# Kernel tuning notes

Hardware: AMD Instinct MI355X
Metric: run time of the kernel (lower is better)

Reference implementation:

```python
import jax, jax.numpy as jnp
import numpy as np
import math

B, S, HID, NH, K_SIG = 8, 8192, 1024, 16, 1024
HD = HID // NH
SCALE = math.sqrt(HD)

def _lin(x, W, b):
    # torch nn.Linear: x @ W.T + b, W is [out, in]
    return jnp.einsum('...i,oi->...o', x, W) + b

def setup_inputs() -> dict:
    key = jax.random.key(0)
    ks = jax.random.split(key, 16)
    hidden_states = jax.random.normal(ks[0], (B, S, HID), jnp.float32)
    # mask with exactly K_SIG ones per row (matches torch padding semantics exactly)
    perm = jax.vmap(lambda k: jax.random.permutation(k, S))(jax.random.split(ks[1], B))
    idx = perm[:, :K_SIG]
    mask = jnp.zeros((B, S), bool).at[jnp.arange(B)[:, None], idx].set(True)
    register_state = jax.random.normal(ks[2], (B, HID), jnp.float32)
    def w(k):
        return jax.random.normal(k, (HID, HID), jnp.float32) * 0.02
    def bvec(k):
        return jax.random.normal(k, (HID,), jnp.float32) * 0.02
    return {
        'hidden_states': hidden_states, 'mask': mask, 'register_state': register_state,
        'Wq': w(ks[3]), 'bq': bvec(ks[4]), 'Wk': w(ks[5]), 'bk': bvec(ks[6]),
        'Wv': w(ks[7]), 'bv': bvec(ks[8]), 'Wo': w(ks[9]), 'bo': bvec(ks[10]),
        'Wrk': w(ks[11]), 'brk': bvec(ks[12]), 'Wrv': w(ks[13]), 'brv': bvec(ks[14]),
    }

def reference(hidden_states, mask, register_state, Wq, bq, Wk, bk, Wv, bv, Wo, bo, Wrk, brk, Wrv, brv):
    # sorted indices of the K_SIG True positions per row (stable argsort puts
    # True (~mask == False) first, in original order)
    idx = jnp.argsort(jnp.logical_not(mask), axis=1, stable=True)[:, :K_SIG]  # [B, K_SIG]
    signal = jnp.take_along_axis(hidden_states, idx[:, :, None], axis=1)      # [B, K_SIG, HID]

    Q = _lin(signal, Wq, bq).reshape(B, K_SIG, NH, HD)
    Kt = _lin(signal, Wk, bk)
    Vt = _lin(signal, Wv, bv)
    Kr = _lin(register_state, Wrk, brk)[:, None, :]
    Vr = _lin(register_state, Wrv, brv)[:, None, :]
    K = jnp.concatenate([Kt, Kr], axis=1).reshape(B, K_SIG + 1, NH, HD)
    V = jnp.concatenate([Vt, Vr], axis=1).reshape(B, K_SIG + 1, NH, HD)

    scores = jnp.einsum('bqhd,bkhd->bhqk', Q, K) / SCALE
    attn = jax.nn.softmax(scores, axis=-1)
    ao = jnp.einsum('bhqk,bkhd->bqhd', attn, V).reshape(B, K_SIG, HID)
    ao = _lin(ao, Wo, bo)

    # scatter back into a copy of hidden_states
    out = hidden_states.at[jnp.arange(B)[:, None], idx].set(ao)
    return out
```

## Files before the change

### kernel.cpp

```cpp
#include <hip/hip_runtime.h>
#include <hip/hip_bf16.h>
#include <math.h>

#define Bc    8
#define Sc    8192
#define HIDc  1024
#define NHc   16
#define HDc   64
#define KSc   1024
#define QSCALE 0.18033688f

typedef __bf16 bf16_t;
typedef __bf16 bf16x8 __attribute__((ext_vector_type(8)));
typedef float  f32x4  __attribute__((ext_vector_type(4)));

#define OFF_IDX   ((size_t)256)
#define OFF_SIG   ((size_t)295168)
#define OFF_WQKV  ((size_t)17072384)
#define OFF_WO    ((size_t)23363840)
#define OFF_QKV   ((size_t)25460992)
#define OFF_KR    ((size_t)75792640)
#define OFF_VR    ((size_t)75809024)
#define OFF_AO    ((size_t)75825408)

__device__ inline void gll16(const bf16_t* g, bf16_t* l) {
  __builtin_amdgcn_global_load_lds(
      (const __attribute__((address_space(1))) void*)g,
      (__attribute__((address_space(3))) void*)l, 16, 0, 0);
}

__global__ __launch_bounds__(256) void front1_kernel(
    const unsigned char* __restrict__ m8, int* __restrict__ idx) {
  __shared__ int shc[256];
  __shared__ int f_sh;
  const int b = blockIdx.x, t = threadIdx.x;
  const unsigned char* raw = m8 + (size_t)b * Sc;
  int c8 = 0;
  for (int i = t; i < Sc; i += 256) c8 += (raw[i] != 0);
  shc[t] = c8;
  __syncthreads();
  for (int s2 = 128; s2 > 0; s2 >>= 1) {
    if (t < s2) shc[t] += shc[t + s2];
    __syncthreads();
  }
  if (t == 0) f_sh = (shc[0] == KSc) ? 1 : 0;
  __syncthreads();
  const int f = f_sh;
  const int* m32 = (const int*)m8;
  const int base = b * Sc + t * 32;
  int c = 0;
  for (int i = 0; i < 32; i++)
    c += f ? (m8[base + i] != 0) : (m32[base + i] != 0);
  shc[t] = c;
  __syncthreads();
  if (t == 0) {
    int run = 0;
    for (int j = 0; j < 256; j++) { int v = shc[j]; shc[j] = run; run += v; }
  }
  __syncthreads();
  int off = b * KSc + shc[t];
  for (int i = 0; i < 32; i++) {
    int on = f ? (m8[base + i] != 0) : (m32[base + i] != 0);
    if (on) { idx[off] = t * 32 + i; off++; }
  }
}

__global__ __launch_bounds__(256) void front2_kernel(
    const float* __restrict__ hidden, const int* __restrict__ idx,
    const float* __restrict__ Wq, const float* __restrict__ Wk,
    const float* __restrict__ Wv, const float* __restrict__ Wo,
    const float* __restrict__ rst,
    const float* __restrict__ Wrk, const float* __restrict__ brk,
    const float* __restrict__ Wrv, const float* __restrict__ brv,
    bf16_t* __restrict__ sig, bf16_t* __restrict__ Wqkv,
    bf16_t* __restrict__ Wob, bf16_t* __restrict__ Krb,
    bf16_t* __restrict__ Vrb) {
  const int bid = blockIdx.x, t = threadIdx.x;
  if (bid < 1024) {
    const int s0 = bid * 8;
    const int b = s0 >> 10;
    float4 v[8];
#pragma unroll
    for (int j = 0; j < 8; j++) {
      const int srow = idx[s0 + j];
      v[j] = *(const float4*)(hidden + ((size_t)b * Sc + srow) * HIDc + t * 4);
    }
#pragma unroll
    for (int j = 0; j < 8; j++) {
      bf16_t* d = sig + (size_t)(s0 + j) * HIDc + t * 4;
      d[0] = (bf16_t)v[j].x; d[1] = (bf16_t)v[j].y;
      d[2] = (bf16_t)v[j].z; d[3] = (bf16_t)v[j].w;
    }
  } else if (bid < 5120) {
    int gid = (bid - 1024) * 256 + t;
    int e4 = gid * 4;
    if (e4 < 3 * 1048576) {
      int sel = e4 >> 20, cc = e4 & 1048575;
      const float* src = sel == 0 ? Wq : (sel == 1 ? Wk : Wv);
      float4 v = *(const float4*)(src + cc);
      bf16_t* d = Wqkv + e4;
      d[0] = (bf16_t)v.x; d[1] = (bf16_t)v.y; d[2] = (bf16_t)v.z; d[3] = (bf16_t)v.w;
    } else {
      int cc = e4 - 3 * 1048576;
      float4 v = *(const float4*)(Wo + cc);
      bf16_t* d = Wob + cc;
      d[0] = (bf16_t)v.x; d[1] = (bf16_t)v.y; d[2] = (bf16_t)v.z; d[3] = (bf16_t)v.w;
    }
  } else {
    const int wid = (bid - 5120) * 4 + (t >> 6);
    const int lane = t & 63;
    const int isV = wid >> 10, j = wid & 1023;
    const float* Wrow = (isV ? Wrv : Wrk) + (size_t)j * HIDc;
    float4 w[4];
#pragma unroll
    for (int i = 0; i < 4; i++) w[i] = ((const float4*)Wrow)[i * 64 + lane];
    const float bias = (isV ? brv : brk)[j];
#pragma unroll
    for (int b = 0; b < 8; b++) {
      const float4* r4 = (const float4*)(rst + (size_t)b * HIDc);
      float s = 0.f;
#pragma unroll
      for (int i = 0; i < 4; i++) {
        float4 r = r4[i * 64 + lane];
        s += w[i].x * r.x + w[i].y * r.y + w[i].z * r.z + w[i].w * r.w;
      }
      s += __shfl_xor(s, 1);  s += __shfl_xor(s, 2);  s += __shfl_xor(s, 4);
      s += __shfl_xor(s, 8);  s += __shfl_xor(s, 16); s += __shfl_xor(s, 32);
      if (lane == 0)
        (isV ? Vrb : Krb)[(size_t)b * HIDc + j] = (bf16_t)(s + bias);
    }
  }
}

__device__ inline void gemm_mainloop(const bf16_t* __restrict__ A,
                                     const bf16_t* __restrict__ Bw,
                                     int tile_m, int tile_n,
                                     bf16_t* As, bf16_t* Bs, f32x4 acc[4][4]) {
  const int t = threadIdx.x, lane = t & 63, w = t >> 6;
  const int wm = w >> 1, wn = w & 1;
  const int r16 = lane & 15, kq = lane >> 4;
  for (int k0 = 0; k0 < 1024; k0 += 32) {
#pragma unroll
    for (int rr = 0; rr < 2; ++rr) {
      int e = rr * 2048 + w * 512 + lane * 8;
      int row = e >> 5, kk = e & 31;
      gll16(A + (size_t)(tile_m + row) * 1024 + k0 + kk, As + rr * 2048 + w * 512);
      gll16(Bw + (size_t)(tile_n + row) * 1024 + k0 + kk, Bs + rr * 2048 + w * 512);
    }
    __syncthreads();
    bf16x8 af[4], bfr[4];
#pragma unroll
    for (int m = 0; m < 4; m++)
      af[m] = *(const bf16x8*)(As + (wm * 64 + m * 16 + r16) * 32 + kq * 8);
#pragma unroll
    for (int n = 0; n < 4; n++)
      bfr[n] = *(const bf16x8*)(Bs + (wn * 64 + n * 16 + r16) * 32 + kq * 8);
#pragma unroll
    for (int m = 0; m < 4; m++)
#pragma unroll
      for (int n = 0; n < 4; n++)
        acc[m][n] = __builtin_amdgcn_mfma_f32_16x16x32_bf16(af[m], bfr[n], acc[m][n], 0, 0, 0);
    __syncthreads();
  }
}

__global__ __launch_bounds__(256) void gemm_qkv_kernel(
    const bf16_t* __restrict__ A, const bf16_t* __restrict__ Bw,
    const float* __restrict__ bq, const float* __restrict__ bk,
    const float* __restrict__ bv, bf16_t* __restrict__ C) {
  __shared__ bf16_t As[128 * 32];
  __shared__ bf16_t Bs[128 * 32];
  const int tile_m = blockIdx.y * 128, tile_n = blockIdx.x * 128;
  f32x4 acc[4][4] = {};
  gemm_mainloop(A, Bw, tile_m, tile_n, As, Bs, acc);
  const int t = threadIdx.x, lane = t & 63, w = t >> 6;
  const int wm = w >> 1, wn = w & 1;
  const int r16 = lane & 15, kq = lane >> 4;
#pragma unroll
  for (int m = 0; m < 4; m++)
#pragma unroll
    for (int n = 0; n < 4; n++) {
      int col = tile_n + wn * 64 + n * 16 + r16;
      int sel = col >> 10, cc = col & 1023;
      float bias = sel == 0 ? bq[cc] : (sel == 1 ? bk[cc] : bv[cc]);
#pragma unroll
      for (int r = 0; r < 4; r++) {
        int row = tile_m + wm * 64 + m * 16 + kq * 4 + r;
        float v = acc[m][n][r] + bias;
        if (sel == 0) v *= QSCALE;
        C[(size_t)row * 3072 + col] = (bf16_t)v;
      }
    }
}

__global__ __launch_bounds__(256) void gemm_ao_kernel(
    const bf16_t* __restrict__ A, const bf16_t* __restrict__ Bw,
    const float* __restrict__ bo, const int* __restrict__ idx,
    float* __restrict__ dout) {
  __shared__ bf16_t As[128 * 32];
  __shared__ bf16_t Bs[128 * 32];
  const int tile_m = blockIdx.y * 128, tile_n = blockIdx.x * 128;
  f32x4 acc[4][4] = {};
  gemm_mainloop(A, Bw, tile_m, tile_n, As, Bs, acc);
  const int t = threadIdx.x, lane = t & 63, w = t >> 6;
  const int wm = w >> 1, wn = w & 1;
  const int r16 = lane & 15, kq = lane >> 4;
#pragma unroll
  for (int m = 0; m < 4; m++)
#pragma unroll
    for (int n = 0; n < 4; n++) {
      int col = tile_n + wn * 64 + n * 16 + r16;
      float bias = bo[col];
#pragma unroll
      for (int r = 0; r < 4; r++) {
        int row = tile_m + wm * 64 + m * 16 + kq * 4 + r;
        float v = acc[m][n][r] + bias;
        int bb = row >> 10;
        int drow = idx[row];
        dout[((size_t)bb * Sc + drow) * HIDc + col] = v;
      }
    }
}

__global__ __launch_bounds__(512) void attn_kernel(
    const bf16_t* __restrict__ QKV, const bf16_t* __restrict__ Krb,
    const bf16_t* __restrict__ Vrb, bf16_t* __restrict__ AO) {
  __shared__ bf16_t Kb[3][4096];
  __shared__ bf16_t Vt[2][4096];
  __shared__ bf16_t Pl[8][2048];
  const int t = threadIdx.x, lane = t & 63, w = t >> 6;
  const int gbk = blockIdx.x;
  const int li = (gbk & 7) * 64 + (gbk >> 3);
  const int qt = li & 3, h = (li >> 2) & 15, b = li >> 6;
  const int r16 = lane & 15, kq = lane >> 4;
  const int qbase = qt * 256 + w * 32;

  const int kK = t >> 3;
  const int dK = ((t & 7) ^ (kK & 7)) * 8;
  const bf16_t* kSrc = QKV + (size_t)(b * KSc + kK) * 3072 + 1024 + h * 64 + dK;
  const int kv8 = t >> 3, dv8 = (t & 7) * 8;
  const int vchunk = kv8 >> 3, voff = kv8 & 7, t7 = t & 7;
  const bf16_t* vSrc = QKV + (size_t)(b * KSc + kv8) * 3072 + 2048 + h * 64 + dv8;

  bf16x8 qf[2][2];
#pragma unroll
  for (int m = 0; m < 2; m++)
#pragma unroll
    for (int kc = 0; kc < 2; kc++)
      qf[m][kc] = *(const bf16x8*)(QKV +
          (size_t)(b * KSc + qbase + m * 16 + r16) * 3072 + h * 64 + kc * 32 + kq * 8);

  f32x4 o[2][4] = {};
  f32x4 osum[2] = {};

  bf16x8 vones;
#pragma unroll
  for (int j = 0; j < 8; j++) vones[j] = (bf16_t)1.0f;

  {
    bf16x8 v0 = *(const bf16x8*)vSrc;
    gll16(kSrc, &Kb[0][w * 512]);
    gll16(kSrc + (size_t)64 * 3072, &Kb[1][w * 512]);
#pragma unroll
    for (int j = 0; j < 8; j++)
      Vt[0][(dv8 + j) * 64 + (((vchunk ^ j ^ t7) << 3) | voff)] = v0[j];
  }
  asm volatile("s_waitcnt vmcnt(1) lgkmcnt(0)" ::: "memory");
  __builtin_amdgcn_s_barrier();

  for (int kt = 0; kt < 17; ++kt) {
    const int cbK = kt % 3;
    const int cbV = kt & 1, nbV = cbV ^ 1;
    bf16x8 vreg = {};
    if (kt < 15) {
      vreg = *(const bf16x8*)(vSrc + (size_t)(kt + 1) * 64 * 3072);
    } else if (kt == 15) {
      if (kv8 == 0) vreg = *(const bf16x8*)(Vrb + (size_t)b * HIDc + h * 64 + dv8);
    }
    if (kt <= 13) {
      gll16(kSrc + (size_t)(kt + 2) * 64 * 3072, &Kb[(kt + 2) % 3][w * 512]);
    } else if (kt == 14) {
      bf16x8 kz = {};
      if (kK == 0) kz = *(const bf16x8*)(Krb + (size_t)b * HIDc + h * 64 + dK);
      *(bf16x8*)(&Kb[1][t * 8]) = kz;
    }
    const bf16_t* Ks = Kb[cbK];

    f32x4 s[2][4] = {};
    __builtin_amdgcn_s_setprio(1);
#pragma unroll
    for (int n = 0; n < 4; n++) {
      const int rowk = n * 16 + r16;
#pragma unroll
      for (int kc = 0; kc < 2; kc++) {
        bf16x8 kf = *(const bf16x8*)(Ks + rowk * 64 +
                                     (((kc * 4 + kq) ^ (rowk & 7)) << 3));
#pragma unroll
        for (int m = 0; m < 2; m++)
          s[m][n] = __builtin_amdgcn_mfma_f32_16x16x32_bf16(kf, qf[m][kc], s[m][n], 0, 0, 0);
      }
    }
    __builtin_amdgcn_s_setprio(0);

    if (kt == 16) {
#pragma unroll
      for (int m = 0; m < 2; m++)
#pragma unroll
        for (int n = 0; n < 4; n++)
#pragma unroll
          for (int r = 0; r < 4; r++)
            if (!(n == 0 && kq == 0 && r == 0)) s[m][n][r] = -1e30f;
    }

    bf16_t* Pw = Pl[w];
#pragma unroll
    for (int m = 0; m < 2; m++)
#pragma unroll
      for (int n = 0; n < 4; n++) {
        float p0 = exp2f(s[m][n][0]), p1 = exp2f(s[m][n][1]);
        float p2 = exp2f(s[m][n][2]), p3 = exp2f(s[m][n][3]);
        unsigned lo, hi;
        asm("v_cvt_pk_bf16_f32 %0, %1, %2" : "=v"(lo) : "v"(p0), "v"(p1));
        asm("v_cvt_pk_bf16_f32 %0, %1, %2" : "=v"(hi) : "v"(p2), "v"(p3));
        unsigned long long pk = (unsigned long long)lo |
                                ((unsigned long long)hi << 32);
        *(unsigned long long*)(Pw + (m * 16 + r16) * 64 +
                               ((n * 16 + kq * 4) ^ ((r16 & 7) << 3))) = pk;
      }

    bf16x8 pa[2][2];
#pragma unroll
    for (int m = 0; m < 2; m++)
#pragma unroll
      for (int kc = 0; kc < 2; kc++)
        pa[m][kc] = *(const bf16x8*)(Pw + (m * 16 + r16) * 64 +
                                     ((kc * 32 + kq * 8) ^ ((r16 & 7) << 3)));

    const bf16_t* Vrow = Vt[cbV];
    __builtin_amdgcn_s_setprio(1);
#pragma unroll
    for (int n = 0; n < 4; n++) {
      const int rowv = n * 16 + r16;
      const int xr = (r16 & 7) ^ ((2 * n + (r16 >> 3)) & 7);
#pragma unroll
      for (int kc = 0; kc < 2; kc++) {
        bf16x8 vb = *(const bf16x8*)(Vrow + rowv * 64 +
                                     (((kc * 4 + kq) ^ xr) << 3));
#pragma unroll
        for (int m = 0; m < 2; m++)
          o[m][n] = __builtin_amdgcn_mfma_f32_16x16x32_bf16(pa[m][kc], vb, o[m][n], 0, 0, 0);
      }
    }
#pragma unroll
    for (int m = 0; m < 2; m++)
#pragma unroll
      for (int kc = 0; kc < 2; kc++)
        osum[m] = __builtin_amdgcn_mfma_f32_16x16x32_bf16(pa[m][kc], vones, osum[m], 0, 0, 0);
    __builtin_amdgcn_s_setprio(0);

    if (kt < 16) {
#pragma unroll
      for (int j = 0; j < 8; j++)
        Vt[nbV][(dv8 + j) * 64 + (((vchunk ^ j ^ t7) << 3) | voff)] = vreg[j];
      asm volatile("s_waitcnt vmcnt(1) lgkmcnt(0)" ::: "memory");
      __builtin_amdgcn_s_barrier();
    }
  }

#pragma unroll
  for (int m = 0; m < 2; m++)
#pragma unroll
    for (int n = 0; n < 4; n++)
#pragma unroll
      for (int r = 0; r < 4; r++) {
        float v = o[m][n][r] / osum[m][r];
        int rowg = b * KSc + qbase + m * 16 + kq * 4 + r;
        int col = h * 64 + n * 16 + r16;
        AO[(size_t)rowg * HIDc + col] = (bf16_t)v;
      }
}

extern "C" void kernel_launch(void* const* d_in, const int* in_sizes, int n_in,
                              void* d_out, int out_size, void* d_ws, size_t ws_size,
                              hipStream_t stream) {
  const float* hidden = (const float*)d_in[0];
  const void*  maskp  = d_in[1];
  const float* rst    = (const float*)d_in[2];
  const float* Wq = (const float*)d_in[3];  const float* bq = (const float*)d_in[4];
  const float* Wk = (const float*)d_in[5];  const float* bk = (const float*)d_in[6];
  const float* Wv = (const float*)d_in[7];  const float* bv = (const float*)d_in[8];
  const float* Wo = (const float*)d_in[9];  const float* bo = (const float*)d_in[10];
  const float* Wrk = (const float*)d_in[11]; const float* brk = (const float*)d_in[12];
  const float* Wrv = (const float*)d_in[13]; const float* brv = (const float*)d_in[14];
  float* dout = (float*)d_out;

  char* ws = (char*)d_ws;
  int*    idx  = (int*)(ws + OFF_IDX);
  bf16_t* sig  = (bf16_t*)(ws + OFF_SIG);
  bf16_t* Wqkv = (bf16_t*)(ws + OFF_WQKV);
  bf16_t* Wob  = (bf16_t*)(ws + OFF_WO);
  bf16_t* QKV  = (bf16_t*)(ws + OFF_QKV);
  bf16_t* Krb  = (bf16_t*)(ws + OFF_KR);
  bf16_t* Vrb  = (bf16_t*)(ws + OFF_VR);
  bf16_t* AO   = (bf16_t*)(ws + OFF_AO);

  hipMemcpyAsync(dout, hidden, (size_t)Bc * Sc * HIDc * sizeof(float),
                 hipMemcpyDeviceToDevice, stream);
  front1_kernel<<<Bc, 256, 0, stream>>>((const unsigned char*)maskp, idx);
  front2_kernel<<<5632, 256, 0, stream>>>(hidden, idx, Wq, Wk, Wv, Wo, rst,
                                          Wrk, brk, Wrv, brv,
                                          sig, Wqkv, Wob, Krb, Vrb);
  gemm_qkv_kernel<<<dim3(24, 64), 256, 0, stream>>>(sig, Wqkv, bq, bk, bv, QKV);
  attn_kernel<<<512, 512, 0, stream>>>(QKV, Krb, Vrb, AO);
  gemm_ao_kernel<<<dim3(8, 64), 256, 0, stream>>>(AO, Wob, bo, idx, dout);
}
```

Measured before the change: 314.2 us.

## Split attention into 256-thread blocks with 128 queries and double-buffered K

Attention blocks shrink from 8 waves over 256 queries to 4 waves over 128 queries, so the grid doubles to 1024 blocks. Each thread now loads two K/V rows per tile, and the K triple buffer becomes a double buffer with a full vmcnt(0) wait each iteration. The aim is more, smaller blocks and less LDS per block so occupancy and load balance improve. In exchange, each K/V tile is loaded by twice as many blocks overall, and the deeper K prefetch is lost.

```diff
diff --git a/kernel.cpp b/kernel.cpp
--- a/kernel.cpp
+++ b/kernel.cpp
@@ -222,25 +222,28 @@
     }
 }
 
-__global__ __launch_bounds__(512) void attn_kernel(
+__global__ __launch_bounds__(256) void attn_kernel(
     const bf16_t* __restrict__ QKV, const bf16_t* __restrict__ Krb,
     const bf16_t* __restrict__ Vrb, bf16_t* __restrict__ AO) {
-  __shared__ bf16_t Kb[3][4096];
+  __shared__ bf16_t Kb[2][4096];
   __shared__ bf16_t Vt[2][4096];
-  __shared__ bf16_t Pl[8][2048];
+  __shared__ bf16_t Pl[4][2048];
   const int t = threadIdx.x, lane = t & 63, w = t >> 6;
   const int gbk = blockIdx.x;
-  const int li = (gbk & 7) * 64 + (gbk >> 3);
-  const int qt = li & 3, h = (li >> 2) & 15, b = li >> 6;
+  const int li = (gbk & 7) * 128 + (gbk >> 3);
+  const int qt = li & 7, h = (li >> 3) & 15, b = li >> 7;
   const int r16 = lane & 15, kq = lane >> 4;
-  const int qbase = qt * 256 + w * 32;
-
-  const int kK = t >> 3;
-  const int dK = ((t & 7) ^ (kK & 7)) * 8;
-  const bf16_t* kSrc = QKV + (size_t)(b * KSc + kK) * 3072 + 1024 + h * 64 + dK;
-  const int kv8 = t >> 3, dv8 = (t & 7) * 8;
-  const int vchunk = kv8 >> 3, voff = kv8 & 7, t7 = t & 7;
-  const bf16_t* vSrc = QKV + (size_t)(b * KSc + kv8) * 3072 + 2048 + h * 64 + dv8;
+  const int qbase = qt * 128 + w * 32;
+
+  const int kK0 = t >> 3;
+  const int dK = ((t & 7) ^ (kK0 & 7)) * 8;
+  const bf16_t* kSrc0 = QKV + (size_t)(b * KSc + kK0) * 3072 + 1024 + h * 64 + dK;
+  const bf16_t* kSrc1 = kSrc0 + (size_t)32 * 3072;
+  const int kv0 = t >> 3, dv8 = (t & 7) * 8;
+  const int vch0 = kv0 >> 3, vof = kv0 & 7, t7 = t & 7;
+  const int vch1 = vch0 + 4;
+  const bf16_t* vSrc0 = QKV + (size_t)(b * KSc + kv0) * 3072 + 2048 + h * 64 + dv8;
+  const bf16_t* vSrc1 = vSrc0 + (size_t)32 * 3072;
 
   bf16x8 qf[2][2];
 #pragma unroll
@@ -258,33 +261,36 @@
   for (int j = 0; j < 8; j++) vones[j] = (bf16_t)1.0f;
 
   {
-    bf16x8 v0 = *(const bf16x8*)vSrc;
-    gll16(kSrc, &Kb[0][w * 512]);
-    gll16(kSrc + (size_t)64 * 3072, &Kb[1][w * 512]);
-#pragma unroll
-    for (int j = 0; j < 8; j++)
-      Vt[0][(dv8 + j) * 64 + (((vchunk ^ j ^ t7) << 3) | voff)] = v0[j];
-  }
-  asm volatile("s_waitcnt vmcnt(1) lgkmcnt(0)" ::: "memory");
+    bf16x8 va = *(const bf16x8*)vSrc0;
+    bf16x8 vb2 = *(const bf16x8*)vSrc1;
+    gll16(kSrc0, &Kb[0][w * 512]);
+    gll16(kSrc1, &Kb[0][2048 + w * 512]);
+#pragma unroll
+    for (int j = 0; j < 8; j++) {
+      Vt[0][(dv8 + j) * 64 + (((vch0 ^ j ^ t7) << 3) | vof)] = va[j];
+      Vt[0][(dv8 + j) * 64 + (((vch1 ^ j ^ t7) << 3) | vof)] = vb2[j];
+    }
+  }
+  asm volatile("s_waitcnt vmcnt(0) lgkmcnt(0)" ::: "memory");
   __builtin_amdgcn_s_barrier();
 
   for (int kt = 0; kt < 17; ++kt) {
-    const int cbK = kt % 3;
-    const int cbV = kt & 1, nbV = cbV ^ 1;
-    bf16x8 vreg = {};
+    const int cb = kt & 1, nb = cb ^ 1;
+    bf16x8 va = {}, vb2 = {};
     if (kt < 15) {
-      vreg = *(const bf16x8*)(vSrc + (size_t)(kt + 1) * 64 * 3072);
+      va  = *(const bf16x8*)(vSrc0 + (size_t)(kt + 1) * 64 * 3072);
+      vb2 = *(const bf16x8*)(vSrc1 + (size_t)(kt + 1) * 64 * 3072);
+      gll16(kSrc0 + (size_t)(kt + 1) * 64 * 3072, &Kb[nb][w * 512]);
+      gll16(kSrc1 + (size_t)(kt + 1) * 64 * 3072, &Kb[nb][2048 + w * 512]);
     } else if (kt == 15) {
-      if (kv8 == 0) vreg = *(const bf16x8*)(Vrb + (size_t)b * HIDc + h * 64 + dv8);
-    }
-    if (kt <= 13) {
-      gll16(kSrc + (size_t)(kt + 2) * 64 * 3072, &Kb[(kt + 2) % 3][w * 512]);
-    } else if (kt == 14) {
+      if (kv0 == 0) va = *(const bf16x8*)(Vrb + (size_t)b * HIDc + h * 64 + dv8);
       bf16x8 kz = {};
-      if (kK == 0) kz = *(const bf16x8*)(Krb + (size_t)b * HIDc + h * 64 + dK);
-      *(bf16x8*)(&Kb[1][t * 8]) = kz;
-    }
-    const bf16_t* Ks = Kb[cbK];
+      if (kK0 == 0) kz = *(const bf16x8*)(Krb + (size_t)b * HIDc + h * 64 + dK);
+      *(bf16x8*)(&Kb[nb][t * 8]) = kz;
+      bf16x8 z = {};
+      *(bf16x8*)(&Kb[nb][(t + 256) * 8]) = z;
+    }
+    const bf16_t* Ks = Kb[cb];
 
     f32x4 s[2][4] = {};
     __builtin_amdgcn_s_setprio(1);
@@ -336,7 +342,7 @@
         pa[m][kc] = *(const bf16x8*)(Pw + (m * 16 + r16) * 64 +
                                      ((kc * 32 + kq * 8) ^ ((r16 & 7) << 3)));
 
-    const bf16_t* Vrow = Vt[cbV];
+    const bf16_t* Vrow = Vt[cb];
     __builtin_amdgcn_s_setprio(1);
 #pragma unroll
     for (int n = 0; n < 4; n++) {
@@ -360,9 +366,11 @@
 
     if (kt < 16) {
 #pragma unroll
-      for (int j = 0; j < 8; j++)
-        Vt[nbV][(dv8 + j) * 64 + (((vchunk ^ j ^ t7) << 3) | voff)] = vreg[j];
-      asm volatile("s_waitcnt vmcnt(1) lgkmcnt(0)" ::: "memory");
+      for (int j = 0; j < 8; j++) {
+        Vt[nb][(dv8 + j) * 64 + (((vch0 ^ j ^ t7) << 3) | vof)] = va[j];
+        Vt[nb][(dv8 + j) * 64 + (((vch1 ^ j ^ t7) << 3) | vof)] = vb2[j];
+      }
+      asm volatile("s_waitcnt vmcnt(0) lgkmcnt(0)" ::: "memory");
       __builtin_amdgcn_s_barrier();
     }
   }
@@ -411,6 +419,6 @@
                                           Wrk, brk, Wrv, brv,
                                           sig, Wqkv, Wob, Krb, Vrb);
   gemm_qkv_kernel<<<dim3(24, 64), 256, 0, stream>>>(sig, Wqkv, bq, bk, bv, QKV);
-  attn_kernel<<<512, 512, 0, stream>>>(QKV, Krb, Vrb, AO);
+  attn_kernel<<<1024, 256, 0, stream>>>(QKV, Krb, Vrb, AO);
   gemm_ao_kernel<<<dim3(8, 64), 256, 0, stream>>>(AO, Wob, bo, idx, dout);
 }
```

Result: no change. 316.3 us (+0.7%).
